# Performance work log

Hardware: AMD Instinct MI355X
Metric: run time of the kernel (lower is better)

Reference implementation:

```python
import jax, jax.numpy as jnp
import numpy as np
import math
from functools import lru_cache

DIM = 64   # num_inputs
HID = 32   # hidden_dim
B = 1024
LOG2 = math.log(2.0)
LOG_2PI = math.log(2.0 * math.pi)


@lru_cache(maxsize=None)
def _masks(out_f, in_f, dim):
    ob, ib = out_f // dim, in_f // dim
    md = np.zeros((out_f, in_f), np.float32)
    mo = np.ones((out_f, in_f), np.float32)
    for i in range(dim):
        md[i * ob:(i + 1) * ob, i * ib:(i + 1) * ib] = 1.0
        mo[i * ob:(i + 1) * ob, i * ib:] = 0.0
    return jnp.asarray(md), jnp.asarray(mo)


def masked_weight(x, grad, W, dw, b, dim):
    # W: (out_f, in_f), dw: (out_f, 1), b: (out_f,)
    out_f, in_f = W.shape
    ob, ib = out_f // dim, in_f // dim
    md, mo = _masks(out_f, in_f, dim)
    w = jnp.exp(W) * md + W * mo                      # positive diag blocks, masked lower blocks
    wsn = jnp.sum(w * w, axis=-1, keepdims=True)      # (out_f, 1) weight-norm denom^2
    wn = jnp.exp(dw) * w / jnp.sqrt(wsn)              # weight-normalized matrix
    wpl = dw + W - 0.5 * jnp.log(wsn)                 # log of diag-block entries, (out_f, in_f)
    # extract diagonal blocks: (dim, ob, dim, ib) -> diag over block index -> (ob, ib, dim)
    blocks = jnp.diagonal(wpl.reshape(dim, ob, dim, ib), axis1=0, axis2=2)
    g = jnp.transpose(blocks, (2, 0, 1))              # (dim, ob, ib) == torch g per-sample
    out = x @ wn.T + b
    if grad is None:
        return out, jnp.broadcast_to(g[None], (x.shape[0],) + g.shape)
    # grad: (Bt, dim, a, c); log-domain block 'matmul' via logsumexp over shared axis a(=ib)
    comb = g[None, :, :, None, :] + jnp.swapaxes(grad, -1, -2)[:, :, None, :, :]  # (Bt,dim,ob,c,ib)
    return out, jax.nn.logsumexp(comb, axis=-1)       # (Bt, dim, ob, c)


def tanh_layer(x, grad):
    g = -2.0 * (x - LOG2 + jax.nn.softplus(-2.0 * x))
    return jnp.tanh(x), g.reshape(grad.shape) + grad


def bnaf_flow(x, p0, p1, p2, gate, dim):
    out, grad = masked_weight(x, None, *p0, dim)
    out, grad = tanh_layer(out, grad)
    out, grad = masked_weight(out, grad, *p1, dim)
    out, grad = tanh_layer(out, grad)
    out, grad = masked_weight(out, grad, *p2, dim)
    g = grad.reshape(grad.shape[0], dim)              # squeeze (B, dim, 1, 1) -> (B, dim)
    if gate is None:
        return out, jnp.sum(g, -1)
    s = jax.nn.sigmoid(gate)
    out = s * out + (1.0 - s) * x
    ldj = jnp.sum(jax.nn.softplus(g + gate) - jax.nn.softplus(gate), -1)
    return out, ldj


def _forward(x, params, gates):
    ldj = 0.0
    for f in range(3):
        gate = gates[f] if f < 2 else None
        x, l = bnaf_flow(x, params[f][0], params[f][1], params[f][2], gate, DIM)
        ldj = ldj + l
        if f < 2:
            x = x[:, ::-1]                            # Permutation('flip'), log-det 0
    log_p_y = jnp.sum(-0.5 * x * x - 0.5 * LOG_2PI, -1)
    return log_p_y + ldj                              # (B,)


def setup_inputs() -> dict:
    key = jax.random.key(0)
    ks = iter(jax.random.split(key, 64))
    d, dh = DIM, DIM * HID
    shapes = [(dh, d), (dh, dh), (d, dh)]
    inp = {"x": jax.random.normal(next(ks), (B, d), jnp.float32)}
    for f in range(3):
        for l, (o, i) in enumerate(shapes):
            inp[f"W{f}_{l}"] = 0.1 * jax.random.normal(next(ks), (o, i), jnp.float32)
            inp[f"dw{f}_{l}"] = jnp.log(jax.random.uniform(next(ks), (o, 1), jnp.float32, 0.1, 1.0))
            inp[f"b{f}_{l}"] = 0.01 * jax.random.normal(next(ks), (o,), jnp.float32)
    inp["gate0"] = jax.random.normal(next(ks), (1,), jnp.float32)
    inp["gate1"] = jax.random.normal(next(ks), (1,), jnp.float32)
    return inp


def reference(x, W0_0, dw0_0, b0_0, W0_1, dw0_1, b0_1, W0_2, dw0_2, b0_2,
              W1_0, dw1_0, b1_0, W1_1, dw1_1, b1_1, W1_2, dw1_2, b1_2,
              W2_0, dw2_0, b2_0, W2_1, dw2_1, b2_1, W2_2, dw2_2, b2_2,
              gate0, gate1):
    params = [
        [(W0_0, dw0_0, b0_0), (W0_1, dw0_1, b0_1), (W0_2, dw0_2, b0_2)],
        [(W1_0, dw1_0, b1_0), (W1_1, dw1_1, b1_1), (W1_2, dw1_2, b1_2)],
        [(W2_0, dw2_0, b2_0), (W2_1, dw2_1, b2_1), (W2_2, dw2_2, b2_2)],
    ]
    return _forward(x, params, (gate0, gate1))
```

## Files before the change

### kernel.cpp

```cpp
#include <hip/hip_runtime.h>
#include <hip/hip_bf16.h>
#include <math.h>


#define DIMN 64
#define BATCH 1024
#define HIDF 2048
#define SPLITK 4
#define NT2 32

typedef __attribute__((ext_vector_type(8))) short short8;
typedef __attribute__((ext_vector_type(4))) float floatx4;
typedef __hip_bfloat16 bf16;

__device__ __forceinline__ float softplusf_(float t) {
    return fmaxf(t, 0.f) + log1pf(__expf(-fabsf(t)));
}

__device__ __forceinline__ float bf2f(short v) {
    union { unsigned u; float f; } x;
    x.u = ((unsigned)(unsigned short)v) << 16;
    return x.f;
}

__device__ __forceinline__ void gl_lds16(const void* g, void* l) {
    __builtin_amdgcn_global_load_lds(
        (const __attribute__((address_space(1))) unsigned int*)g,
        (__attribute__((address_space(3))) unsigned int*)l, 16, 0, 0);
}

__device__ __forceinline__ void tanh_sech2_(float p, float& th, float& s2) {
    float t = __expf(-2.f * fabsf(p));
    float opt = 1.f + t;
    float inv = 1.f / opt;
    th = copysignf((1.f - t) * inv, p);
    s2 = 4.f * t * inv * inv;
}

template<int INF>
__device__ __forceinline__ void prep_row(
    const float* __restrict__ W, const float* __restrict__ dw,
    void* __restrict__ wn_out, float* __restrict__ eg,
    int r, int lane, int out_f, int ob, int ib, int transpose, int bf16out)
{
    constexpr int NI = INF / 64;
    int d = r / ob;
    int c0 = d * ib;
    int c1 = c0 + ib;
    const float* Wr = W + (size_t)r * INF;

    float vv[NI];
    float ss = 0.f;
#pragma unroll
    for (int i = 0; i < NI; ++i) {
        int c = lane + i * 64;
        float wraw = Wr[c];
        float wv = (c < c0) ? wraw : ((c < c1) ? __expf(wraw) : 0.f);
        vv[i] = wv;
        ss += wv * wv;
    }
    for (int off = 32; off > 0; off >>= 1) ss += __shfl_xor(ss, off, 64);

    float dwr = dw[r];
    float scale = __expf(dwr) / sqrtf(ss);
    float logt = dwr - 0.5f * __logf(ss);

#pragma unroll
    for (int i = 0; i < NI; ++i) {
        int c = lane + i * 64;
        float val = scale * vv[i];
        if (bf16out) {
            ((bf16*)wn_out)[(size_t)r * INF + c] = __float2bfloat16(val);
        } else if (transpose) {
            ((float*)wn_out)[(size_t)c * out_f + r] = val;
        } else {
            ((float*)wn_out)[(size_t)r * INF + c] = val;
        }
    }
    if (lane < ib) eg[(size_t)r * ib + lane] = __expf(logt + Wr[c0 + lane]);
}

struct PrepIn { const float *W0, *dw0, *W1, *dw1, *W2, *dw2; };

__global__ __launch_bounds__(256) void prep_mega(
    PrepIn p0, PrepIn p1, PrepIn p2,
    float* __restrict__ wn0T_all, float* __restrict__ eg0_all,
    bf16* __restrict__ wn1_all, float* __restrict__ e1_all,
    bf16* __restrict__ wn2b_all, float* __restrict__ e2_all)
{
    int blk = blockIdx.x;
    int wave = threadIdx.x >> 6;
    int lane = threadIdx.x & 63;
    int f = blk / 1040;
    int rem = blk - f * 1040;
    int rr = rem * 4 + wave;
    PrepIn P = (f == 0) ? p0 : ((f == 1) ? p1 : p2);

    float* wn0T = wn0T_all + (size_t)f * DIMN * HIDF;
    float* eg0  = eg0_all  + (size_t)f * HIDF;
    bf16* wn1   = wn1_all + (size_t)f * HIDF * HIDF;
    float* e1   = e1_all   + (size_t)f * HIDF * 32;
    bf16* wn2b  = wn2b_all + (size_t)f * DIMN * HIDF;
    float* e2   = e2_all   + (size_t)f * DIMN * 32;

    if (rr < HIDF) {
        prep_row<DIMN>(P.W0, P.dw0, wn0T, eg0, rr, lane, HIDF, 32, 1, 1, 0);
    } else if (rr < 2 * HIDF) {
        prep_row<HIDF>(P.W1, P.dw1, wn1, e1, rr - HIDF, lane, HIDF, 32, 32, 0, 1);
    } else {
        prep_row<HIDF>(P.W2, P.dw2, wn2b, e2, rr - 2 * HIDF, lane, DIMN, 1, 32, 0, 1);
    }
}

__global__ __launch_bounds__(256) void gemm0_act(
    const float* __restrict__ xin, const float* __restrict__ wn0T,
    const float* __restrict__ bias, const float* __restrict__ eg0,
    bf16* __restrict__ h0, bf16* __restrict__ g0e)
{
    __shared__ float xs[16][DIMN];
    int b0 = blockIdx.y * 16;
    {
        const float4* src = (const float4*)(xin + (size_t)b0 * DIMN);
        ((float4*)xs)[threadIdx.x] = src[threadIdx.x];
    }
    __syncthreads();
    int n = blockIdx.x * 256 + threadIdx.x;

    float acc[16];
#pragma unroll
    for (int j = 0; j < 16; ++j) acc[j] = 0.f;

#pragma unroll 4
    for (int c4 = 0; c4 < 16; ++c4) {
        int c = c4 * 4;
        float w0 = wn0T[(size_t)(c + 0) * HIDF + n];
        float w1 = wn0T[(size_t)(c + 1) * HIDF + n];
        float w2 = wn0T[(size_t)(c + 2) * HIDF + n];
        float w3 = wn0T[(size_t)(c + 3) * HIDF + n];
#pragma unroll
        for (int j = 0; j < 16; ++j) {
            float4 x4 = *(const float4*)&xs[j][c];
            acc[j] = fmaf(x4.x, w0, acc[j]);
            acc[j] = fmaf(x4.y, w1, acc[j]);
            acc[j] = fmaf(x4.z, w2, acc[j]);
            acc[j] = fmaf(x4.w, w3, acc[j]);
        }
    }
    float bv = bias[n], egv = eg0[n];
#pragma unroll
    for (int j = 0; j < 16; ++j) {
        float p = acc[j] + bv;
        float th, s2;
        tanh_sech2_(p, th, s2);
        size_t idx = (size_t)(b0 + j) * HIDF + n;
        h0[idx] = __float2bfloat16(th);
        g0e[idx] = __float2bfloat16(egv * s2);
    }
}

__constant__ unsigned char G1_JN[40] = {
    3,4,5,6,7,7,8,8,9,9,10,10,11,11,11,12,12,12,13,13,13,14,14,14,
    15,15,15,15, 2,6,10,14, 1,5,9,13, 0,4,8,12 };
__constant__ unsigned char G1_KZ[40] = {
    0,0,0,0,0,1,0,1,0,1, 0, 1, 0, 1, 2, 0, 1, 2, 0, 1, 2, 0, 1, 2,
     0, 1, 2, 3, 0,1, 2, 3, 0,1,2,3, 0,1,2,3 };

#define G1BK 64
__global__ __launch_bounds__(256) void gemm1_part(
    const bf16* __restrict__ A, const bf16* __restrict__ B,
    bf16* __restrict__ part)
{
    const int K = HIDF, N = HIDF;
    int pr = blockIdx.x >> 3;
    int my = blockIdx.x & 7;
    int jn = G1_JN[pr];
    int kz = G1_KZ[pr];
    int kbase = kz * (K / SPLITK);
    int kend = (jn + 1) * 128 - kbase;
    if (kend > K / SPLITK) kend = K / SPLITK;

    __shared__ short As[128 * 64];
    __shared__ short Bs[128 * 64];
    int tid = threadIdx.x;
    int lane = tid & 63;
    int wave = tid >> 6;
    int n0 = jn * 128;
    int m0 = my * 128;
    int wr = wave >> 1;
    int wc = wave & 1;
    int rf = lane & 15;
    int q = lane >> 4;

    const char* agp[4];
    const char* bgp[4];
    char* alds[4];
    char* blds[4];
#pragma unroll
    for (int s = 0; s < 4; ++s) {
        int c = tid + s * 256;
        int row = c >> 3;
        int kc = (c & 7) ^ (row & 7);
        agp[s] = (const char*)A + ((size_t)(m0 + row) * K + kbase) * 2 + kc * 16;
        bgp[s] = (const char*)B + ((size_t)(n0 + row) * K + kbase) * 2 + kc * 16;
        alds[s] = (char*)As + c * 16;
        blds[s] = (char*)Bs + c * 16;
    }

    floatx4 acc[4][4];
#pragma unroll
    for (int i = 0; i < 4; ++i)
#pragma unroll
        for (int j = 0; j < 4; ++j) acc[i][j] = (floatx4){0.f, 0.f, 0.f, 0.f};

    int rowA0 = wr * 64 + rf;
    int rowB0 = wc * 64 + rf;

    for (int k0 = 0; k0 < kend; k0 += G1BK) {
        size_t kb = (size_t)k0 * 2;
        __syncthreads();
#pragma unroll
        for (int s = 0; s < 4; ++s) {
            gl_lds16(agp[s] + kb, alds[s]);
            gl_lds16(bgp[s] + kb, blds[s]);
        }
        __syncthreads();

#pragma unroll
        for (int s = 0; s < 2; ++s) {
            short8 af[4], bfv[4];
#pragma unroll
            for (int i = 0; i < 4; ++i) {
                int row = rowA0 + i * 16;
                af[i] = *(const short8*)&As[row * 64 + (((s * 4 + q) ^ (row & 7)) * 8)];
            }
#pragma unroll
            for (int j = 0; j < 4; ++j) {
                int row = rowB0 + j * 16;
                bfv[j] = *(const short8*)&Bs[row * 64 + (((s * 4 + q) ^ (row & 7)) * 8)];
            }
#pragma unroll
            for (int i = 0; i < 4; ++i)
#pragma unroll
                for (int j = 0; j < 4; ++j)
                    acc[i][j] = __builtin_amdgcn_mfma_f32_16x16x32_bf16(af[i], bfv[j], acc[i][j], 0, 0, 0);
        }
    }

    bf16* pk = part + (size_t)kz * BATCH * HIDF;
    int col = lane & 15;
    int rq = (lane >> 4) * 4;
#pragma unroll
    for (int i = 0; i < 4; ++i) {
#pragma unroll
        for (int j = 0; j < 4; ++j) {
            int n = n0 + wc * 64 + j * 16 + col;
#pragma unroll
            for (int r = 0; r < 4; ++r) {
                int m = m0 + wr * 64 + i * 16 + rq + r;
                pk[(size_t)m * N + n] = __float2bfloat16(acc[i][j][r]);
            }
        }
    }
}

__global__ __launch_bounds__(256) void act_grad_gemm2(
    const bf16* __restrict__ part, const float* __restrict__ bias,
    const float* __restrict__ e1, const bf16* __restrict__ g0e,
    const bf16* __restrict__ wn2b,
    bf16* __restrict__ grad1e, float* __restrict__ out2p)
{
    __shared__ char smem[17408 + 8704 + 8192];
    float* g0s = (float*)smem;
    short* h1s = (short*)(smem + 17408);
    short* Bs2 = (short*)(smem + 17408 + 8704);

    int tid = threadIdx.x;
    int lane = tid & 63;
    int wave = tid >> 6;
    int bx = blockIdx.x;
    int n0 = bx * 64;
    int b0 = blockIdx.y * 64;
    int np = (bx >> 3) + 1;

    {
        int c0c = tid, c1c = tid + 256;
        int r0 = c0c >> 3, k0c = (c0c & 7) ^ (r0 & 7);
        int r1 = c1c >> 3, k1c = (c1c & 7) ^ (r1 & 7);
        gl_lds16((const char*)wn2b + ((size_t)r0 * HIDF + n0) * 2 + k0c * 16,
                 (char*)Bs2 + c0c * 16);
        gl_lds16((const char*)wn2b + ((size_t)r1 * HIDF + n0) * 2 + k1c * 16,
                 (char*)Bs2 + c1c * 16);
    }

    for (int s = tid; s < 512; s += 256) {
        int row = s >> 3, c8 = s & 7;
        short8 v = *(const short8*)((const short*)g0e +
                                    (size_t)(b0 + row) * HIDF + n0 + c8 * 8);
        float4 lo = { bf2f(v[0]), bf2f(v[1]), bf2f(v[2]), bf2f(v[3]) };
        float4 hi = { bf2f(v[4]), bf2f(v[5]), bf2f(v[6]), bf2f(v[7]) };
        *(float4*)&g0s[row * 68 + c8 * 8] = lo;
        *(float4*)&g0s[row * 68 + c8 * 8 + 4] = hi;
    }

    int g = tid >> 6;
    int nl = tid & 63;
    int n = n0 + nl;

    float4 er[8];
    const float4* e1r = (const float4*)(e1 + (size_t)n * 32);
#pragma unroll
    for (int qq = 0; qq < 8; ++qq) er[qq] = e1r[qq];

    float bv = bias[n];
    int kb2 = nl & 32;
    const bf16* pp0 = part;
    const bf16* pp1 = (np > 1) ? part + (size_t)1 * BATCH * HIDF : part;
    const bf16* pp2 = (np > 2) ? part + (size_t)2 * BATCH * HIDF : part;
    const bf16* pp3 = (np > 3) ? part + (size_t)3 * BATCH * HIDF : part;
    float m1 = (np > 1) ? 1.f : 0.f;
    float m2 = (np > 2) ? 1.f : 0.f;
    float m3 = (np > 3) ? 1.f : 0.f;

    __syncthreads();

#pragma unroll
    for (int t = 0; t < 16; ++t) {
        int bl = g * 16 + t;
        int b = b0 + bl;
        size_t idx = (size_t)b * HIDF + n;
        float l0 = __bfloat162float(pp0[idx]);
        float l1 = __bfloat162float(pp1[idx]);
        float l2 = __bfloat162float(pp2[idx]);
        float l3 = __bfloat162float(pp3[idx]);
        float pre = bv + l0;
        pre = fmaf(m1, l1, pre);
        pre = fmaf(m2, l2, pre);
        pre = fmaf(m3, l3, pre);
        float th, s2;
        tanh_sech2_(pre, th, s2);
        const float* g0row = &g0s[bl * 68 + kb2];
        float dot = 0.f;
#pragma unroll
        for (int qq = 0; qq < 8; ++qq) {
            float4 gv = *(const float4*)&g0row[qq * 4];
            dot = fmaf(gv.x, er[qq].x, dot);
            dot = fmaf(gv.y, er[qq].y, dot);
            dot = fmaf(gv.z, er[qq].z, dot);
            dot = fmaf(gv.w, er[qq].w, dot);
        }
        bf16 thb = __float2bfloat16(th);
        h1s[bl * 68 + nl] = *(const short*)&thb;
        grad1e[idx] = __float2bfloat16(dot * s2);
    }
    __syncthreads();

    int rf = lane & 15;
    int q = lane >> 4;
    floatx4 acc2[4];
#pragma unroll
    for (int j = 0; j < 4; ++j) acc2[j] = (floatx4){0.f, 0.f, 0.f, 0.f};

#pragma unroll
    for (int s = 0; s < 2; ++s) {
        int rowa = wave * 16 + rf;
        short8 af = *(const short8*)&h1s[rowa * 68 + s * 32 + q * 8];
#pragma unroll
        for (int j = 0; j < 4; ++j) {
            int rowb = j * 16 + rf;
            int cp = (s * 4 + q) ^ (rowb & 7);
            short8 bfv = *(const short8*)&Bs2[rowb * 64 + cp * 8];
            acc2[j] = __builtin_amdgcn_mfma_f32_16x16x32_bf16(af, bfv, acc2[j], 0, 0, 0);
        }
    }

    float* outk = out2p + (size_t)bx * BATCH * DIMN;
    int col = lane & 15;
    int rq = (lane >> 4) * 4;
#pragma unroll
    for (int j = 0; j < 4; ++j) {
#pragma unroll
        for (int r = 0; r < 4; ++r) {
            int m = b0 + wave * 16 + rq + r;
            outk[(size_t)m * DIMN + j * 16 + col] = acc2[j][r];
        }
    }
}

__global__ __launch_bounds__(256) void tail_gemm0(
    const float* __restrict__ out2p, const float* __restrict__ b2,
    const float* __restrict__ e2, const bf16* __restrict__ grad1e,
    const float* __restrict__ x_cur, const float* __restrict__ gate,
    float* __restrict__ x_next, float* __restrict__ ldj, int accum_ldj,
    const float* __restrict__ wn0T_n, const float* __restrict__ bias_n,
    const float* __restrict__ eg0_n,
    bf16* __restrict__ h0, bf16* __restrict__ g0e)
{
    __shared__ float xs[16][DIMN];
    int tid = threadIdx.x;
    int bx = blockIdx.x;
    int b0 = blockIdx.y * 16;
    int n = tid & 63;
    int rowg = tid >> 6;

    float gt = gate[0];
    float sg = 1.f / (1.f + __expf(-gt));
    float bv2 = b2[n];

#pragma unroll
    for (int i = 0; i < 4; ++i) {
        int row = rowg * 4 + i;
        int b = b0 + row;
        float o = bv2;
#pragma unroll
        for (int p = 0; p < NT2; ++p)
            o += out2p[(size_t)p * BATCH * DIMN + (size_t)b * DIMN + n];
        float xo = sg * o + (1.f - sg) * x_cur[(size_t)b * DIMN + n];
        xs[row][63 - n] = xo;

        if (bx == 0) {
            x_next[(size_t)b * DIMN + (63 - n)] = xo;
            const short8* gr = (const short8*)((const short*)grad1e +
                                               (size_t)b * HIDF + n * 32);
            const float4* gc = (const float4*)(e2 + n * 32);
            float s = 0.f;
#pragma unroll
            for (int q = 0; q < 4; ++q) {
                short8 a8 = gr[q];
                float4 c0 = gc[2 * q], c1 = gc[2 * q + 1];
                s = fmaf(bf2f(a8[0]), c0.x, s);
                s = fmaf(bf2f(a8[1]), c0.y, s);
                s = fmaf(bf2f(a8[2]), c0.z, s);
                s = fmaf(bf2f(a8[3]), c0.w, s);
                s = fmaf(bf2f(a8[4]), c1.x, s);
                s = fmaf(bf2f(a8[5]), c1.y, s);
                s = fmaf(bf2f(a8[6]), c1.z, s);
                s = fmaf(bf2f(a8[7]), c1.w, s);
            }
            float gF = __logf(fmaxf(s, 1e-45f));
            float contrib = softplusf_(gF + gt) - softplusf_(gt);
            for (int off = 32; off > 0; off >>= 1)
                contrib += __shfl_xor(contrib, off, 64);
            if (n == 0) ldj[b] = accum_ldj ? (ldj[b] + contrib) : contrib;
        }
    }
    __syncthreads();

    int nn = bx * 256 + tid;

    float acc[16];
#pragma unroll
    for (int j = 0; j < 16; ++j) acc[j] = 0.f;

#pragma unroll 4
    for (int c4 = 0; c4 < 16; ++c4) {
        int c = c4 * 4;
        float w0 = wn0T_n[(size_t)(c + 0) * HIDF + nn];
        float w1 = wn0T_n[(size_t)(c + 1) * HIDF + nn];
        float w2 = wn0T_n[(size_t)(c + 2) * HIDF + nn];
        float w3 = wn0T_n[(size_t)(c + 3) * HIDF + nn];
#pragma unroll
        for (int j = 0; j < 16; ++j) {
            float4 x4 = *(const float4*)&xs[j][c];
            acc[j] = fmaf(x4.x, w0, acc[j]);
            acc[j] = fmaf(x4.y, w1, acc[j]);
            acc[j] = fmaf(x4.z, w2, acc[j]);
            acc[j] = fmaf(x4.w, w3, acc[j]);
        }
    }
    float bvn = bias_n[nn], egv = eg0_n[nn];
#pragma unroll
    for (int j = 0; j < 16; ++j) {
        float p = acc[j] + bvn;
        float th, s2;
        tanh_sech2_(p, th, s2);
        size_t idx = (size_t)(b0 + j) * HIDF + nn;
        h0[idx] = __float2bfloat16(th);
        g0e[idx] = __float2bfloat16(egv * s2);
    }
}

__global__ __launch_bounds__(256) void tail_final(
    const float* __restrict__ out2p, const float* __restrict__ b2,
    const float* __restrict__ e2, const bf16* __restrict__ grad1e,
    const float* __restrict__ ldj, float* __restrict__ out)
{
    int tid = threadIdx.x;
    int b = blockIdx.x * 4 + (tid >> 6);
    int n = tid & 63;

    float o = b2[n];
#pragma unroll
    for (int p = 0; p < NT2; ++p)
        o += out2p[(size_t)p * BATCH * DIMN + (size_t)b * DIMN + n];

    const short8* gr = (const short8*)((const short*)grad1e + (size_t)b * HIDF + n * 32);
    const float4* gc = (const float4*)(e2 + n * 32);
    float s = 0.f;
#pragma unroll
    for (int q = 0; q < 4; ++q) {
        short8 a8 = gr[q];
        float4 c0 = gc[2 * q], c1 = gc[2 * q + 1];
        s = fmaf(bf2f(a8[0]), c0.x, s);
        s = fmaf(bf2f(a8[1]), c0.y, s);
        s = fmaf(bf2f(a8[2]), c0.z, s);
        s = fmaf(bf2f(a8[3]), c0.w, s);
        s = fmaf(bf2f(a8[4]), c1.x, s);
        s = fmaf(bf2f(a8[5]), c1.y, s);
        s = fmaf(bf2f(a8[6]), c1.z, s);
        s = fmaf(bf2f(a8[7]), c1.w, s);
    }
    float gF = __logf(fmaxf(s, 1e-45f));

    float contrib = gF - 0.5f * o * o - 0.91893853320467274f;
    for (int off = 32; off > 0; off >>= 1) contrib += __shfl_xor(contrib, off, 64);
    if (n == 0) out[b] = ldj[b] + contrib;
}

extern "C" void kernel_launch(void* const* d_in, const int* in_sizes, int n_in,
                              void* d_out, int out_size, void* d_ws, size_t ws_size,
                              hipStream_t stream)
{
    (void)in_sizes; (void)n_in; (void)out_size; (void)ws_size;

    const float* x = (const float*)d_in[0];
    const float* gates[2] = { (const float*)d_in[28], (const float*)d_in[29] };

    char* ws = (char*)d_ws;
    size_t ofs = 0;
    auto alloc = [&](size_t bytes) { char* p = ws + ofs; ofs += (bytes + 255) & ~(size_t)255; return p; };

    bf16* wn1_all  = (bf16*)alloc((size_t)3 * HIDF * HIDF * 2);
    bf16* wn2b_all = (bf16*)alloc((size_t)3 * DIMN * HIDF * 2);
    float* wn0T_all = (float*)alloc((size_t)3 * DIMN * HIDF * 4);
    float* eg0_all  = (float*)alloc((size_t)3 * HIDF * 4);
    float* e1_all   = (float*)alloc((size_t)3 * HIDF * 32 * 4);
    float* e2_all   = (float*)alloc((size_t)3 * DIMN * 32 * 4);
    bf16* h0   = (bf16*)alloc((size_t)BATCH * HIDF * 2);
    bf16* part = (bf16*)alloc((size_t)SPLITK * BATCH * HIDF * 2);
    bf16* g0e    = (bf16*)alloc((size_t)BATCH * HIDF * 2);
    bf16* grad1e = (bf16*)alloc((size_t)BATCH * HIDF * 2);
    float* out2p  = (float*)alloc((size_t)NT2 * BATCH * DIMN * 4);
    float* x1     = (float*)alloc((size_t)BATCH * DIMN * 4);
    float* x2     = (float*)alloc((size_t)BATCH * DIMN * 4);
    float* ldj    = (float*)alloc(BATCH * 4);
    float* outp   = (float*)d_out;

    auto W = [&](int f, int i) { return (const float*)d_in[1 + f * 9 + i]; };

    PrepIn p0 = { W(0,0), W(0,1), W(0,3), W(0,4), W(0,6), W(0,7) };
    PrepIn p1 = { W(1,0), W(1,1), W(1,3), W(1,4), W(1,6), W(1,7) };
    PrepIn p2 = { W(2,0), W(2,1), W(2,3), W(2,4), W(2,6), W(2,7) };

    prep_mega<<<dim3(3 * 1040), dim3(256), 0, stream>>>(
        p0, p1, p2, wn0T_all, eg0_all, wn1_all, e1_all, wn2b_all, e2_all);

    gemm0_act<<<dim3(8, BATCH / 16), dim3(256), 0, stream>>>(
        x, wn0T_all, W(0,2), eg0_all, h0, g0e);

    const float* xcur = x;
    float* xnexts[2] = { x1, x2 };

    for (int f = 0; f < 3; ++f) {
        size_t fo1 = (size_t)f * HIDF * HIDF;
        size_t fo2 = (size_t)f * DIMN * HIDF;

        gemm1_part<<<dim3(320), dim3(256), 0, stream>>>(
            h0, wn1_all + fo1, part);

        act_grad_gemm2<<<dim3(HIDF / 64, BATCH / 64), dim3(256), 0, stream>>>(
            part, W(f,5), e1_all + (size_t)f * HIDF * 32, g0e,
            wn2b_all + fo2, grad1e, out2p);

        if (f < 2) {
            tail_gemm0<<<dim3(8, BATCH / 16), dim3(256), 0, stream>>>(
                out2p, W(f,8), e2_all + (size_t)f * DIMN * 32, grad1e,
                xcur, gates[f], xnexts[f], ldj, f,
                wn0T_all + (size_t)(f + 1) * DIMN * HIDF, W(f + 1, 2),
                eg0_all + (size_t)(f + 1) * HIDF, h0, g0e);
            xcur = xnexts[f];
        } else {
            tail_final<<<dim3(BATCH / 4), dim3(256), 0, stream>>>(
                out2p, W(2,8), e2_all + (size_t)2 * DIMN * 32, grad1e, ldj, outp);
        }
    }
}
```

Measured before the change: 308.1 us.

## Split tail into separate transform and gemm0 kernels; vectorize weight prep rows

The fused tail_gemm0 kernel, which recomputed the split-K reduction of out2p in each of its 8 column blocks before running the next flow's first layer, is split in two. A lightweight tail_trans kernel does the reduction, gating and log-det once per row, and the existing gemm0_act kernel is then launched on the new x. This removes the eightfold redundant reduction at the cost of one extra launch and a round-trip of x through global memory. The prep kernel is also specialized: the first layer gets a single-column path, and wide rows use float4 loads with packed bf16 stores.

Measured after the change: 285.2 us. 1.08x faster.

```diff
diff --git a/kernel.cpp b/kernel.cpp
--- a/kernel.cpp
+++ b/kernel.cpp
@@ -21,6 +21,11 @@
     union { unsigned u; float f; } x;
     x.u = ((unsigned)(unsigned short)v) << 16;
     return x.f;
+}
+
+__device__ __forceinline__ short f2bf_s(float f) {
+    bf16 b = __float2bfloat16(f);
+    return *(short*)&b;
 }
 
 __device__ __forceinline__ void gl_lds16(const void* g, void* l) {
@@ -37,27 +42,49 @@
     s2 = 4.f * t * inv * inv;
 }
 
-template<int INF>
-__device__ __forceinline__ void prep_row(
+__device__ __forceinline__ void prep_row0(
     const float* __restrict__ W, const float* __restrict__ dw,
-    void* __restrict__ wn_out, float* __restrict__ eg,
-    int r, int lane, int out_f, int ob, int ib, int transpose, int bf16out)
-{
-    constexpr int NI = INF / 64;
-    int d = r / ob;
-    int c0 = d * ib;
-    int c1 = c0 + ib;
-    const float* Wr = W + (size_t)r * INF;
-
-    float vv[NI];
+    float* __restrict__ wn0T, float* __restrict__ eg0, int r, int lane)
+{
+    int d = r >> 5;
+    const float* Wr = W + (size_t)r * 64;
+    float wraw = Wr[lane];
+    float wv = (lane < d) ? wraw : ((lane == d) ? __expf(wraw) : 0.f);
+    float ss = wv * wv;
+    for (int off = 32; off > 0; off >>= 1) ss += __shfl_xor(ss, off, 64);
+    float dwr = dw[r];
+    float scale = __expf(dwr) / sqrtf(ss);
+    wn0T[(size_t)lane * HIDF + r] = scale * wv;
+    if (lane == 0) eg0[r] = __expf(dwr - 0.5f * __logf(ss) + Wr[d]);
+}
+
+__device__ __forceinline__ void prep_row_wide(
+    const float* __restrict__ W, const float* __restrict__ dw,
+    bf16* __restrict__ wn, float* __restrict__ eg,
+    int r, int lane, int d)
+{
+    int c0 = d * 32, c1 = c0 + 32;
+    const float* Wr = W + (size_t)r * 2048;
+
+    float4 va[4], vb[4];
     float ss = 0.f;
 #pragma unroll
-    for (int i = 0; i < NI; ++i) {
-        int c = lane + i * 64;
-        float wraw = Wr[c];
-        float wv = (c < c0) ? wraw : ((c < c1) ? __expf(wraw) : 0.f);
-        vv[i] = wv;
-        ss += wv * wv;
+    for (int i = 0; i < 4; ++i) {
+        int cb = i * 512 + lane * 8;
+        float4 a = *(const float4*)&Wr[cb];
+        float4 b = *(const float4*)&Wr[cb + 4];
+        a.x = (cb + 0 < c0) ? a.x : ((cb + 0 < c1) ? __expf(a.x) : 0.f);
+        a.y = (cb + 1 < c0) ? a.y : ((cb + 1 < c1) ? __expf(a.y) : 0.f);
+        a.z = (cb + 2 < c0) ? a.z : ((cb + 2 < c1) ? __expf(a.z) : 0.f);
+        a.w = (cb + 3 < c0) ? a.w : ((cb + 3 < c1) ? __expf(a.w) : 0.f);
+        b.x = (cb + 4 < c0) ? b.x : ((cb + 4 < c1) ? __expf(b.x) : 0.f);
+        b.y = (cb + 5 < c0) ? b.y : ((cb + 5 < c1) ? __expf(b.y) : 0.f);
+        b.z = (cb + 6 < c0) ? b.z : ((cb + 6 < c1) ? __expf(b.z) : 0.f);
+        b.w = (cb + 7 < c0) ? b.w : ((cb + 7 < c1) ? __expf(b.w) : 0.f);
+        va[i] = a;
+        vb[i] = b;
+        ss += a.x * a.x + a.y * a.y + a.z * a.z + a.w * a.w
+            + b.x * b.x + b.y * b.y + b.z * b.z + b.w * b.w;
     }
     for (int off = 32; off > 0; off >>= 1) ss += __shfl_xor(ss, off, 64);
 
@@ -66,18 +93,20 @@
     float logt = dwr - 0.5f * __logf(ss);
 
 #pragma unroll
-    for (int i = 0; i < NI; ++i) {
-        int c = lane + i * 64;
-        float val = scale * vv[i];
-        if (bf16out) {
-            ((bf16*)wn_out)[(size_t)r * INF + c] = __float2bfloat16(val);
-        } else if (transpose) {
-            ((float*)wn_out)[(size_t)c * out_f + r] = val;
-        } else {
-            ((float*)wn_out)[(size_t)r * INF + c] = val;
-        }
-    }
-    if (lane < ib) eg[(size_t)r * ib + lane] = __expf(logt + Wr[c0 + lane]);
+    for (int i = 0; i < 4; ++i) {
+        float4 a = va[i], b = vb[i];
+        short8 pk;
+        pk[0] = f2bf_s(scale * a.x);
+        pk[1] = f2bf_s(scale * a.y);
+        pk[2] = f2bf_s(scale * a.z);
+        pk[3] = f2bf_s(scale * a.w);
+        pk[4] = f2bf_s(scale * b.x);
+        pk[5] = f2bf_s(scale * b.y);
+        pk[6] = f2bf_s(scale * b.z);
+        pk[7] = f2bf_s(scale * b.w);
+        *(short8*)((short*)wn + (size_t)r * 2048 + i * 512 + lane * 8) = pk;
+    }
+    if (lane < 32) eg[(size_t)r * 32 + lane] = __expf(logt + Wr[c0 + lane]);
 }
 
 struct PrepIn { const float *W0, *dw0, *W1, *dw1, *W2, *dw2; };
@@ -104,11 +133,13 @@
     float* e2   = e2_all   + (size_t)f * DIMN * 32;
 
     if (rr < HIDF) {
-        prep_row<DIMN>(P.W0, P.dw0, wn0T, eg0, rr, lane, HIDF, 32, 1, 1, 0);
+        prep_row0(P.W0, P.dw0, wn0T, eg0, rr, lane);
     } else if (rr < 2 * HIDF) {
-        prep_row<HIDF>(P.W1, P.dw1, wn1, e1, rr - HIDF, lane, HIDF, 32, 32, 0, 1);
+        int r = rr - HIDF;
+        prep_row_wide(P.W1, P.dw1, wn1, e1, r, lane, r >> 5);
     } else {
-        prep_row<HIDF>(P.W2, P.dw2, wn2b, e2, rr - 2 * HIDF, lane, DIMN, 1, 32, 0, 1);
+        int r = rr - 2 * HIDF;
+        prep_row_wide(P.W2, P.dw2, wn2b, e2, r, lane, r);
     }
 }
 
@@ -386,97 +417,46 @@
     }
 }
 
-__global__ __launch_bounds__(256) void tail_gemm0(
+__global__ __launch_bounds__(256) void tail_trans(
     const float* __restrict__ out2p, const float* __restrict__ b2,
     const float* __restrict__ e2, const bf16* __restrict__ grad1e,
     const float* __restrict__ x_cur, const float* __restrict__ gate,
-    float* __restrict__ x_next, float* __restrict__ ldj, int accum_ldj,
-    const float* __restrict__ wn0T_n, const float* __restrict__ bias_n,
-    const float* __restrict__ eg0_n,
-    bf16* __restrict__ h0, bf16* __restrict__ g0e)
-{
-    __shared__ float xs[16][DIMN];
+    float* __restrict__ x_next, float* __restrict__ ldj, int accum_ldj)
+{
     int tid = threadIdx.x;
-    int bx = blockIdx.x;
-    int b0 = blockIdx.y * 16;
+    int b = blockIdx.x * 4 + (tid >> 6);
     int n = tid & 63;
-    int rowg = tid >> 6;
+
+    float o = b2[n];
+#pragma unroll
+    for (int p = 0; p < NT2; ++p)
+        o += out2p[(size_t)p * BATCH * DIMN + (size_t)b * DIMN + n];
 
     float gt = gate[0];
     float sg = 1.f / (1.f + __expf(-gt));
-    float bv2 = b2[n];
-
-#pragma unroll
-    for (int i = 0; i < 4; ++i) {
-        int row = rowg * 4 + i;
-        int b = b0 + row;
-        float o = bv2;
-#pragma unroll
-        for (int p = 0; p < NT2; ++p)
-            o += out2p[(size_t)p * BATCH * DIMN + (size_t)b * DIMN + n];
-        float xo = sg * o + (1.f - sg) * x_cur[(size_t)b * DIMN + n];
-        xs[row][63 - n] = xo;
-
-        if (bx == 0) {
-            x_next[(size_t)b * DIMN + (63 - n)] = xo;
-            const short8* gr = (const short8*)((const short*)grad1e +
-                                               (size_t)b * HIDF + n * 32);
-            const float4* gc = (const float4*)(e2 + n * 32);
-            float s = 0.f;
-#pragma unroll
-            for (int q = 0; q < 4; ++q) {
-                short8 a8 = gr[q];
-                float4 c0 = gc[2 * q], c1 = gc[2 * q + 1];
-                s = fmaf(bf2f(a8[0]), c0.x, s);
-                s = fmaf(bf2f(a8[1]), c0.y, s);
-                s = fmaf(bf2f(a8[2]), c0.z, s);
-                s = fmaf(bf2f(a8[3]), c0.w, s);
-                s = fmaf(bf2f(a8[4]), c1.x, s);
-                s = fmaf(bf2f(a8[5]), c1.y, s);
-                s = fmaf(bf2f(a8[6]), c1.z, s);
-                s = fmaf(bf2f(a8[7]), c1.w, s);
-            }
-            float gF = __logf(fmaxf(s, 1e-45f));
-            float contrib = softplusf_(gF + gt) - softplusf_(gt);
-            for (int off = 32; off > 0; off >>= 1)
-                contrib += __shfl_xor(contrib, off, 64);
-            if (n == 0) ldj[b] = accum_ldj ? (ldj[b] + contrib) : contrib;
-        }
-    }
-    __syncthreads();
-
-    int nn = bx * 256 + tid;
-
-    float acc[16];
-#pragma unroll
-    for (int j = 0; j < 16; ++j) acc[j] = 0.f;
-
-#pragma unroll 4
-    for (int c4 = 0; c4 < 16; ++c4) {
-        int c = c4 * 4;
-        float w0 = wn0T_n[(size_t)(c + 0) * HIDF + nn];
-        float w1 = wn0T_n[(size_t)(c + 1) * HIDF + nn];
-        float w2 = wn0T_n[(size_t)(c + 2) * HIDF + nn];
-        float w3 = wn0T_n[(size_t)(c + 3) * HIDF + nn];
-#pragma unroll
-        for (int j = 0; j < 16; ++j) {
-            float4 x4 = *(const float4*)&xs[j][c];
-            acc[j] = fmaf(x4.x, w0, acc[j]);
-            acc[j] = fmaf(x4.y, w1, acc[j]);
-            acc[j] = fmaf(x4.z, w2, acc[j]);
-            acc[j] = fmaf(x4.w, w3, acc[j]);
-        }
-    }
-    float bvn = bias_n[nn], egv = eg0_n[nn];
-#pragma unroll
-    for (int j = 0; j < 16; ++j) {
-        float p = acc[j] + bvn;
-        float th, s2;
-        tanh_sech2_(p, th, s2);
-        size_t idx = (size_t)(b0 + j) * HIDF + nn;
-        h0[idx] = __float2bfloat16(th);
-        g0e[idx] = __float2bfloat16(egv * s2);
-    }
+    float xo = sg * o + (1.f - sg) * x_cur[(size_t)b * DIMN + n];
+    x_next[(size_t)b * DIMN + (63 - n)] = xo;
+
+    const short8* gr = (const short8*)((const short*)grad1e + (size_t)b * HIDF + n * 32);
+    const float4* gc = (const float4*)(e2 + n * 32);
+    float s = 0.f;
+#pragma unroll
+    for (int q = 0; q < 4; ++q) {
+        short8 a8 = gr[q];
+        float4 c0 = gc[2 * q], c1 = gc[2 * q + 1];
+        s = fmaf(bf2f(a8[0]), c0.x, s);
+        s = fmaf(bf2f(a8[1]), c0.y, s);
+        s = fmaf(bf2f(a8[2]), c0.z, s);
+        s = fmaf(bf2f(a8[3]), c0.w, s);
+        s = fmaf(bf2f(a8[4]), c1.x, s);
+        s = fmaf(bf2f(a8[5]), c1.y, s);
+        s = fmaf(bf2f(a8[6]), c1.z, s);
+        s = fmaf(bf2f(a8[7]), c1.w, s);
+    }
+    float gF = __logf(fmaxf(s, 1e-45f));
+    float contrib = softplusf_(gF + gt) - softplusf_(gt);
+    for (int off = 32; off > 0; off >>= 1) contrib += __shfl_xor(contrib, off, 64);
+    if (n == 0) ldj[b] = accum_ldj ? (ldj[b] + contrib) : contrib;
 }
 
 __global__ __launch_bounds__(256) void tail_final(
@@ -572,11 +552,14 @@
             wn2b_all + fo2, grad1e, out2p);
 
         if (f < 2) {
-            tail_gemm0<<<dim3(8, BATCH / 16), dim3(256), 0, stream>>>(
+            tail_trans<<<dim3(BATCH / 4), dim3(256), 0, stream>>>(
                 out2p, W(f,8), e2_all + (size_t)f * DIMN * 32, grad1e,
-                xcur, gates[f], xnexts[f], ldj, f,
-                wn0T_all + (size_t)(f + 1) * DIMN * HIDF, W(f + 1, 2),
+                xcur, gates[f], xnexts[f], ldj, f);
+
+            gemm0_act<<<dim3(8, BATCH / 16), dim3(256), 0, stream>>>(
+                xnexts[f], wn0T_all + (size_t)(f + 1) * DIMN * HIDF, W(f + 1, 2),
                 eg0_all + (size_t)(f + 1) * HIDF, h0, g0e);
+
             xcur = xnexts[f];
         } else {
             tail_final<<<dim3(BATCH / 4), dim3(256), 0, stream>>>(
```
